# Performance work log

Hardware: AMD Instinct MI355X
Metric: run time of the kernel (lower is better)

## Reference

```python
import jax, jax.numpy as jnp
import numpy as np

T, B, S, H, E, V = 100, 64, 602, 1024, 512, 10000


def setup_inputs() -> dict:
    key = jax.random.key(0)
    ks = jax.random.split(key, 12)
    s = 0.02  # small init scale for numerical stability through tanh/sigmoid
    return {
        "tgt": jax.random.randint(ks[0], (T, B, 1), 0, V),
        "memory_bank": jax.random.normal(ks[1], (S, B, H), jnp.float32),
        "h0": jax.random.normal(ks[2], (2, B, H), jnp.float32) * 0.1,
        "c0": jax.random.normal(ks[3], (2, B, H), jnp.float32) * 0.1,
        "embedding": jax.random.normal(ks[4], (V, E), jnp.float32) * s,
        "Wi0": jax.random.normal(ks[5], (4 * H, E + H), jnp.float32) * s,
        "Wh0": jax.random.normal(ks[6], (4 * H, H), jnp.float32) * s,
        "bi0": jnp.zeros((4 * H,), jnp.float32),
        "bh0": jnp.zeros((4 * H,), jnp.float32),
        "Wi1": jax.random.normal(ks[7], (4 * H, H), jnp.float32) * s,
        "Wh1": jax.random.normal(ks[8], (4 * H, H), jnp.float32) * s,
        "bi1": jnp.zeros((4 * H,), jnp.float32),
        "bh1": jnp.zeros((4 * H,), jnp.float32),
        "W_attn": jax.random.normal(ks[9], (H, H), jnp.float32) * s,
        "W_out": jax.random.normal(ks[10], (H, 2 * H), jnp.float32) * s,
    }


def _lstm_cell(x, h, c, Wi, Wh, bi, bh):
    # PyTorch LSTM gate order: i, f, g, o
    g = x @ Wi.T + h @ Wh.T + bi + bh
    i, f, gg, o = jnp.split(g, 4, axis=-1)
    c2 = jax.nn.sigmoid(f) * c + jax.nn.sigmoid(i) * jnp.tanh(gg)
    h2 = jax.nn.sigmoid(o) * jnp.tanh(c2)
    return h2, c2


def reference(tgt, memory_bank, h0, c0, embedding, Wi0, Wh0, bi0, bh0,
              Wi1, Wh1, bi1, bh1, W_attn, W_out):
    emb = embedding[tgt[:, :, 0]]            # [T, B, E]
    M = jnp.transpose(memory_bank, (1, 0, 2))  # [B, S, H]

    def step(carry, e_t):
        hl0, hl1, cl0, cl1, feed = carry
        x = jnp.concatenate([e_t, feed], axis=-1)        # input feeding
        nh0, nc0 = _lstm_cell(x, hl0, cl0, Wi0, Wh0, bi0, bh0)
        nh1, nc1 = _lstm_cell(nh0, hl1, cl1, Wi1, Wh1, bi1, bh1)
        # GlobalAttention 'general': score = (h W) . m
        q = nh1 @ W_attn.T                                # [B, H]
        align = jnp.einsum('bh,bsh->bs', q, M)            # [B, S]
        a = jax.nn.softmax(align, axis=-1)
        ctx = jnp.einsum('bs,bsh->bh', a, M)              # [B, H]
        out = jnp.tanh(jnp.concatenate([ctx, nh1], -1) @ W_out.T)  # attn_h
        return (nh0, nh1, nc0, nc1, out), (out, a)

    init = (h0[0], h0[1], c0[0], c0[1], jnp.zeros((B, H), emb.dtype))
    (_, _, _, _, _), (outs, attns) = jax.lax.scan(step, init, emb)
    return outs, attns  # [T,B,H], [T,B,S]
```

## Files before the change

kernel.cpp:

```cpp
#include <hip/hip_runtime.h>


#define DI __device__ __forceinline__

typedef __attribute__((ext_vector_type(4))) short s4v;
typedef __attribute__((ext_vector_type(8))) short s8v;
typedef __attribute__((ext_vector_type(4))) float f4v;

DI float b2f(short u) {
  unsigned int x = ((unsigned int)(unsigned short)u) << 16;
  float f; __builtin_memcpy(&f, &x, 4); return f;
}
DI short f2b(float f) {
  unsigned int x; __builtin_memcpy(&x, &f, 4);
  return (short)((x + 0x7fffu + ((x >> 16) & 1u)) >> 16);
}
DI s8v cat8(s4v lo, s4v hi) {
  s8v r; r[0]=lo[0];r[1]=lo[1];r[2]=lo[2];r[3]=lo[3];
  r[4]=hi[0];r[5]=hi[1];r[6]=hi[2];r[7]=hi[3]; return r;
}
DI f4v mfma16(s8v a, s8v b, f4v c) {
  return __builtin_amdgcn_mfma_f32_16x16x32_bf16(a, b, c, 0, 0, 0);
}
DI float sigm(float x) { return 1.f / (1.f + __expf(-x)); }

DI unsigned long long ld64c(const void* p) {
  return __hip_atomic_load((const unsigned long long*)p, __ATOMIC_RELAXED,
                           __HIP_MEMORY_SCOPE_SYSTEM);
}
DI void st64c(void* p, unsigned long long v) {
  __hip_atomic_store((unsigned long long*)p, v, __ATOMIC_RELAXED,
                     __HIP_MEMORY_SCOPE_SYSTEM);
}
DI float ldfc(const float* p) {
  return __hip_atomic_load(p, __ATOMIC_RELAXED, __HIP_MEMORY_SCOPE_SYSTEM);
}
DI void stfc(float* p, float v) {
  __hip_atomic_store(p, v, __ATOMIC_RELAXED, __HIP_MEMORY_SCOPE_SYSTEM);
}
DI void st16c(short* p, short v) {
  asm volatile("global_store_short %0, %1, off sc0 sc1"
               :: "v"(p), "v"((unsigned int)(unsigned short)v) : "memory");
}
union U64S { unsigned long long u; short s[4]; };
union U64F { unsigned long long u; float f[2]; };


__global__ void cvt_bf16(const float* __restrict__ src, short* __restrict__ dst, long n8) {
  long i = (long)blockIdx.x * blockDim.x + threadIdx.x;
  long stride = (long)gridDim.x * blockDim.x;
  for (; i < n8; i += stride) {
    const float* s = src + i * 8;
    s8v o;
    #pragma unroll
    for (int j = 0; j < 8; ++j) o[j] = f2b(s[j]);
    *(s8v*)(dst + i * 8) = o;
  }
}

__global__ void pack_w(const float* __restrict__ WA, int Ka,
                       const float* __restrict__ WB, int Kb,
                       short* __restrict__ dst, int N, long total) {
  long i = (long)blockIdx.x * blockDim.x + threadIdx.x;
  long stride = (long)gridDim.x * blockDim.x;
  for (; i < total; i += stride) {
    int c = (int)(i & 3);
    long r = i >> 2;
    int n = (int)(r % N);
    int kt = (int)(r / N);
    int k = kt * 32 + c * 8;
    const float* s = (k < Ka) ? (WA + (size_t)n * Ka + k)
                              : (WB + (size_t)n * Kb + (k - Ka));
    s8v o;
    #pragma unroll
    for (int j = 0; j < 8; ++j) o[j] = f2b(s[j]);
    *(s8v*)(dst + r * 32 + c * 8) = o;
  }
}

__global__ __launch_bounds__(64) void emb_gather(const int* __restrict__ tgt,
                                                 const float* __restrict__ emb,
                                                 short* __restrict__ dst) {
  int tb = blockIdx.x;
  int idx = tgt[tb];
  const float* s = emb + (size_t)idx * 512 + threadIdx.x * 8;
  s8v o;
  #pragma unroll
  for (int j = 0; j < 8; ++j) o[j] = f2b(s[j]);
  *(s8v*)(dst + (size_t)tb * 512 + threadIdx.x * 8) = o;
}

__global__ void init_state(const float* __restrict__ h0, const float* __restrict__ c0,
                           short* __restrict__ h0r, short* __restrict__ h1r,
                           float* __restrict__ c0buf, float* __restrict__ c1buf,
                           short* __restrict__ feedr) {
  int i = blockIdx.x * 256 + threadIdx.x;
  if (i < 65536) {
    h0r[i] = f2b(h0[i]);
    h1r[i] = f2b(h0[65536 + i]);
    c0buf[i] = c0[i];
    c1buf[i] = c0[65536 + i];
    feedr[i] = 0;
  }
}


template <int K>
DI void stageA(short* As, int rt,
               const short* __restrict__ A0, int ld0, int K0,
               const short* __restrict__ A1, int ld1, int K1,
               const short* __restrict__ A2, int ld2) {
  const int KP = K + 8;
  const int CH = K / 8;
  const int TOT = 16 * CH;
  for (int c = threadIdx.x; c < TOT; c += 256) {
    int row = c / CH, kc = c - row * CH;
    int k = kc * 8;
    int gr = rt * 16 + row;
    const short* p;
    if (k < K0)            p = A0 + (size_t)gr * ld0 + k;
    else if (k < K0 + K1)  p = A1 + (size_t)gr * ld1 + (k - K0);
    else                   p = A2 + (size_t)gr * ld2 + (k - K0 - K1);
    *(s8v*)&As[row * KP + k] = *(const s8v*)p;
  }
}

template <int NG>
DI void kloopL(const short* As, int KP, int k0, int nkt,
               const short* __restrict__ Wp, size_t wkt,
               f4v* acc, int r15, int g) {
  const short* arow = As + r15 * KP + 4 * g;
  #pragma unroll 4
  for (int kt = 0; kt < nkt; ++kt) {
    const short* ap = arow + (k0 + kt) * 32;
    s8v a = cat8(*(const s4v*)ap, *(const s4v*)(ap + 16));
    const short* bp = Wp + (size_t)(k0 + kt) * wkt;
    #pragma unroll
    for (int t = 0; t < NG; ++t)
      acc[t] = mfma16(a, cat8(*(const s4v*)(bp + (size_t)t * 32768),
                              *(const s4v*)(bp + (size_t)t * 32768 + 16)),
                      acc[t]);
  }
}

template <int NG>
DI void wave_reduce(f4v* acc, float* smem, int w, int l) {
  #pragma unroll
  for (int t4 = 0; t4 < NG; ++t4)
    *(f4v*)&smem[(w * 64 + l) * 20 + t4 * 4] = acc[t4];
  __syncthreads();
  if (w == 0) {
    #pragma unroll
    for (int t4 = 0; t4 < NG; ++t4) {
      f4v s0 = *(f4v*)&smem[l * 20 + t4 * 4];
      #pragma unroll
      for (int ww = 1; ww < 4; ++ww) {
        f4v v = *(f4v*)&smem[(ww * 64 + l) * 20 + t4 * 4];
        #pragma unroll
        for (int j = 0; j < 4; ++j) s0[j] += v[j];
      }
      acc[t4] = s0;
    }
  }
}


DI void gbar(int* bar, int bid, int want) {
  __syncthreads();
  if (threadIdx.x == 0) {
    int* leaf = bar + (bid >> 4) * 64;
    if (__hip_atomic_fetch_add(leaf, 1, __ATOMIC_RELAXED,
                               __HIP_MEMORY_SCOPE_AGENT) == want * 16 - 1) {
      if (__hip_atomic_fetch_add(bar + 1024, 1, __ATOMIC_RELAXED,
                                 __HIP_MEMORY_SCOPE_AGENT) == want * 16 - 1) {
        __hip_atomic_store(bar + 1088, want, __ATOMIC_RELAXED,
                           __HIP_MEMORY_SCOPE_AGENT);
      }
    }
    while (__hip_atomic_load(bar + 1088, __ATOMIC_RELAXED,
                             __HIP_MEMORY_SCOPE_AGENT) < want)
      __builtin_amdgcn_s_sleep(2);
  }
  __syncthreads();
}


__global__ __launch_bounds__(256, 1) void decoder_k(
    const short* __restrict__ W0p, const short* __restrict__ W1p,
    const short* __restrict__ Wop, const short* __restrict__ Wap,
    const short* __restrict__ emba,
    const float* __restrict__ bi0, const float* __restrict__ bh0,
    const float* __restrict__ bi1, const float* __restrict__ bh1,
    short* h0r, short* h1r, short* feedr, short* ctxr, short* qb,
    float* c0b, float* c1b, float* alg, float* part,
    const short* __restrict__ Mb, const float* __restrict__ memf,
    float* out, int useMb, int* bar) {
  __shared__ float smem[5248];
  __shared__ __align__(16) short As[16 * 2568];
  const int bid = blockIdx.x, tid = threadIdx.x;
  const int w = tid >> 6, l = tid & 63, r15 = l & 15, g = l >> 4;
  const int cs = bid & 63, rt = bid >> 6;
  int barno = 0;
  f4v z = {0.f, 0.f, 0.f, 0.f};

  for (int t = 0; t < 100; ++t) {
    const size_t scur = (size_t)t * 65536, snxt = (size_t)(t + 1) * 65536;

    {
      f4v acc[4] = {z, z, z, z};
      stageA<2560>(As, rt, emba + (size_t)t * 64 * 512, 512, 512,
                   feedr + scur, 1024, 1024, h0r + scur, 1024);
      __syncthreads();
      const short* wbase = W0p + (size_t)(cs * 16 + r15) * 32 + 4 * g;
      kloopL<4>(As, 2568, w * 20, 20, wbase, (size_t)4096 * 32, acc, r15, g);
      wave_reduce<4>(acc, smem, w, l);
      if (w == 0) {
        int h = cs * 16 + r15;
        float bs0 = bi0[h] + bh0[h];
        float bs1 = bi0[1024 + h] + bh0[1024 + h];
        float bs2 = bi0[2048 + h] + bh0[2048 + h];
        float bs3 = bi0[3072 + h] + bh0[3072 + h];
        #pragma unroll
        for (int q = 0; q < 4; ++q) {
          int brow = rt * 16 + g * 4 + q;
          size_t off = (size_t)brow * 1024 + h;
          float iv = acc[0][q] + bs0, fv = acc[1][q] + bs1;
          float gv = acc[2][q] + bs2, ov = acc[3][q] + bs3;
          float cn = sigm(fv) * c0b[off] + sigm(iv) * tanhf(gv);
          float hn = sigm(ov) * tanhf(cn);
          c0b[off] = cn;
          st16c(h0r + snxt + off, f2b(hn));
        }
      }
      gbar(bar, bid, ++barno);
    }

    {
      f4v acc[4] = {z, z, z, z};
      stageA<2048>(As, rt, h0r + snxt, 1024, 1024, h1r + scur, 1024, 1024,
                   (const short*)nullptr, 0);
      __syncthreads();
      const short* wbase = W1p + (size_t)(cs * 16 + r15) * 32 + 4 * g;
      kloopL<4>(As, 2056, w * 16, 16, wbase, (size_t)4096 * 32, acc, r15, g);
      wave_reduce<4>(acc, smem, w, l);
      if (w == 0) {
        int h = cs * 16 + r15;
        float bs0 = bi1[h] + bh1[h];
        float bs1 = bi1[1024 + h] + bh1[1024 + h];
        float bs2 = bi1[2048 + h] + bh1[2048 + h];
        float bs3 = bi1[3072 + h] + bh1[3072 + h];
        #pragma unroll
        for (int q = 0; q < 4; ++q) {
          int brow = rt * 16 + g * 4 + q;
          size_t off = (size_t)brow * 1024 + h;
          float iv = acc[0][q] + bs0, fv = acc[1][q] + bs1;
          float gv = acc[2][q] + bs2, ov = acc[3][q] + bs3;
          float cn = sigm(fv) * c1b[off] + sigm(iv) * tanhf(gv);
          float hn = sigm(ov) * tanhf(cn);
          c1b[off] = cn;
          st16c(h1r + snxt + off, f2b(hn));
        }
      }
      gbar(bar, bid, ++barno);
    }

    {
      f4v acc[1] = {z};
      stageA<1024>(As, rt, h1r + snxt, 1024, 1024,
                   (const short*)nullptr, 0, 0, (const short*)nullptr, 0);
      __syncthreads();
      const short* wbase = Wap + (size_t)(cs * 16 + r15) * 32 + 4 * g;
      kloopL<1>(As, 1032, w * 8, 8, wbase, (size_t)1024 * 32, acc, r15, g);
      wave_reduce<1>(acc, smem, w, l);
      if (w == 0) {
        int nb = cs * 16 + r15;
        #pragma unroll
        for (int q = 0; q < 4; ++q) {
          int brow = rt * 16 + g * 4 + q;
          st16c(qb + (size_t)brow * 1024 + nb, f2b(acc[0][q]));
        }
      }
      gbar(bar, bid, ++barno);
    }

    {
      int b = bid & 63, chunk = bid >> 6;
      int s0 = chunk * 151;
      int send = 602 < s0 + 151 ? 602 : s0 + 151;
      const short* qp = qb + (size_t)b * 1024 + l * 16;
      float qf[16];
      #pragma unroll
      for (int c4 = 0; c4 < 4; ++c4) {
        U64S x; x.u = ld64c(qp + c4 * 4);
        #pragma unroll
        for (int j = 0; j < 4; ++j) qf[c4 * 4 + j] = b2f(x.s[j]);
      }
      float o[16];
      #pragma unroll
      for (int j = 0; j < 16; ++j) o[j] = 0.f;
      for (int s = s0 + w; s < send; s += 8) {
        int s2 = s + 4;
        bool has2 = s2 < send;
        float mv0[16], mv1[16];
        if (useMb) {
          const short* mp0 = Mb + ((size_t)s * 64 + b) * 1024 + l * 16;
          s8v a0 = *(const s8v*)mp0, a1 = *(const s8v*)(mp0 + 8);
          const short* mp1 = Mb + ((size_t)(has2 ? s2 : s) * 64 + b) * 1024 + l * 16;
          s8v b0 = *(const s8v*)mp1, b1 = *(const s8v*)(mp1 + 8);
          #pragma unroll
          for (int j = 0; j < 8; ++j) {
            mv0[j] = b2f(a0[j]); mv0[8 + j] = b2f(a1[j]);
            mv1[j] = b2f(b0[j]); mv1[8 + j] = b2f(b1[j]);
          }
        } else {
          const float* mp0 = memf + ((size_t)s * 64 + b) * 1024 + l * 16;
          const float* mp1 = memf + ((size_t)(has2 ? s2 : s) * 64 + b) * 1024 + l * 16;
          f4v a0 = *(const f4v*)mp0, a1 = *(const f4v*)(mp0 + 4);
          f4v a2 = *(const f4v*)(mp0 + 8), a3 = *(const f4v*)(mp0 + 12);
          f4v b0 = *(const f4v*)mp1, b1 = *(const f4v*)(mp1 + 4);
          f4v b2 = *(const f4v*)(mp1 + 8), b3 = *(const f4v*)(mp1 + 12);
          #pragma unroll
          for (int j = 0; j < 4; ++j) {
            mv0[j] = a0[j]; mv0[4 + j] = a1[j]; mv0[8 + j] = a2[j]; mv0[12 + j] = a3[j];
            mv1[j] = b0[j]; mv1[4 + j] = b1[j]; mv1[8 + j] = b2[j]; mv1[12 + j] = b3[j];
          }
        }
        float d0 = 0.f, d1 = 0.f;
        #pragma unroll
        for (int j = 0; j < 16; ++j) { d0 += qf[j] * mv0[j]; d1 += qf[j] * mv1[j]; }
        #pragma unroll
        for (int off = 32; off; off >>= 1) {
          d0 += __shfl_down(d0, off);
          d1 += __shfl_down(d1, off);
        }
        d0 = __shfl(d0, 0); d1 = __shfl(d1, 0);
        if (l == 0) {
          stfc(alg + b * 602 + s, d0);
          if (has2) stfc(alg + b * 602 + s2, d1);
        }
        float p0 = __expf(fminf(d0, 80.f) - 8.f);
        float p1 = has2 ? __expf(fminf(d1, 80.f) - 8.f) : 0.f;
        #pragma unroll
        for (int j = 0; j < 16; ++j) o[j] += p0 * mv0[j] + p1 * mv1[j];
      }
      float* pp = part + (size_t)(b * 16 + chunk * 4 + w) * 1024;
      #pragma unroll
      for (int j4 = 0; j4 < 8; ++j4) {
        U64F x; x.f[0] = o[j4 * 2]; x.f[1] = o[j4 * 2 + 1];
        st64c(pp + l * 16 + j4 * 2, x.u);
      }
      gbar(bar, bid, ++barno);
    }

    if (bid < 64) {
      int b = bid;
      float* pv = smem;
      float* red = smem + 604;
      const float* al = alg + b * 602;
      float lm = -1e30f;
      for (int i = tid; i < 602; i += 256) {
        float v = ldfc(al + i); pv[i] = v; lm = fmaxf(lm, v);
      }
      #pragma unroll
      for (int o = 32; o; o >>= 1) lm = fmaxf(lm, __shfl_down(lm, o));
      if (l == 0) red[w] = lm;
      __syncthreads();
      float M = fmaxf(fmaxf(red[0], red[1]), fmaxf(red[2], red[3]));
      float ls = 0.f;
      for (int i = tid; i < 602; i += 256) { float e = __expf(pv[i] - M); pv[i] = e; ls += e; }
      #pragma unroll
      for (int o = 32; o; o >>= 1) ls += __shfl_down(ls, o);
      __syncthreads();
      if (l == 0) red[4 + w] = ls;
      __syncthreads();
      float L = red[4] + red[5] + red[6] + red[7];
      float scale = __expf(8.f - M) / L;
      {
        int h = tid * 4;
        f4v a2 = {0.f, 0.f, 0.f, 0.f};
        #pragma unroll
        for (int p = 0; p < 16; ++p) {
          const float* pr = part + (size_t)(b * 16 + p) * 1024 + h;
          U64F x0, x1; x0.u = ld64c(pr); x1.u = ld64c(pr + 2);
          a2[0] += x0.f[0]; a2[1] += x0.f[1];
          a2[2] += x1.f[0]; a2[3] += x1.f[1];
        }
        U64S ov;
        #pragma unroll
        for (int j = 0; j < 4; ++j) ov.s[j] = f2b(a2[j] * scale);
        st64c(ctxr + snxt + (size_t)b * 1024 + (size_t)tid * 4, ov.u);
      }
      float invL = 1.f / L;
      float* attns = out + 6553600 + (size_t)t * 64 * 602;
      for (int i = tid; i < 602; i += 256) attns[b * 602 + i] = pv[i] * invL;
    }
    gbar(bar, bid, ++barno);

    {
      f4v acc[1] = {z};
      stageA<2048>(As, rt, ctxr + snxt, 1024, 1024, h1r + snxt, 1024, 1024,
                   (const short*)nullptr, 0);
      __syncthreads();
      const short* wbase = Wop + (size_t)(cs * 16 + r15) * 32 + 4 * g;
      kloopL<1>(As, 2056, w * 16, 16, wbase, (size_t)1024 * 32, acc, r15, g);
      wave_reduce<1>(acc, smem, w, l);
      if (w == 0) {
        int nb = cs * 16 + r15;
        float* outp = out + (size_t)t * 65536;
        #pragma unroll
        for (int q = 0; q < 4; ++q) {
          int brow = rt * 16 + g * 4 + q;
          size_t off = (size_t)brow * 1024 + nb;
          float v = tanhf(acc[0][q]);
          outp[off] = v;
          st16c(feedr + snxt + off, f2b(v));
        }
      }
      gbar(bar, bid, ++barno);
    }
  }
}


extern "C" void kernel_launch(void* const* d_in, const int* in_sizes, int n_in,
                              void* d_out, int out_size, void* d_ws, size_t ws_size,
                              hipStream_t stream) {
  const int*   tgt  = (const int*)  d_in[0];
  const float* mem  = (const float*)d_in[1];
  const float* h0   = (const float*)d_in[2];
  const float* c0   = (const float*)d_in[3];
  const float* embw = (const float*)d_in[4];
  const float* Wi0  = (const float*)d_in[5];
  const float* Wh0  = (const float*)d_in[6];
  const float* bi0  = (const float*)d_in[7];
  const float* bh0  = (const float*)d_in[8];
  const float* Wi1  = (const float*)d_in[9];
  const float* Wh1  = (const float*)d_in[10];
  const float* bi1  = (const float*)d_in[11];
  const float* bh1  = (const float*)d_in[12];
  const float* Wat  = (const float*)d_in[13];
  const float* Wou  = (const float*)d_in[14];
  float* out = (float*)d_out;

  char* base = (char*)d_ws;
  size_t off = 0;
  auto alloc = [&](size_t bytes) -> void* {
    void* p = base + off;
    off += (bytes + 255) & ~(size_t)255;
    return p;
  };
  const size_t RING = (size_t)101 * 65536;
  int* bar = (int*)alloc(8192);
  short* qb   = (short*)alloc(65536 * 2);
  float* c0b  = (float*)alloc(65536 * 4);
  float* c1b  = (float*)alloc(65536 * 4);
  float* alg  = (float*)alloc((size_t)64 * 602 * 4);
  float* part = (float*)alloc((size_t)64 * 16 * 1024 * 4);
  short* emba = (short*)alloc((size_t)100 * 64 * 512 * 2);
  short* Wap  = (short*)alloc((size_t)32 * 1024 * 32 * 2);
  short* Wop  = (short*)alloc((size_t)64 * 1024 * 32 * 2);
  short* W1p  = (short*)alloc((size_t)64 * 4096 * 32 * 2);
  short* W0p  = (short*)alloc((size_t)80 * 4096 * 32 * 2);
  short* h0r  = (short*)alloc(RING * 2);
  short* h1r  = (short*)alloc(RING * 2);
  short* feedr= (short*)alloc(RING * 2);
  short* ctxr = (short*)alloc(RING * 2);
  const size_t MBE = (size_t)602 * 64 * 1024;
  bool useMb = (off + MBE * 2 + 256) <= ws_size;
  short* Mb = useMb ? (short*)alloc(MBE * 2) : nullptr;

  hipMemsetAsync(bar, 0, 8192, stream);
  hipLaunchKernelGGL(emb_gather, dim3(6400), dim3(64), 0, stream, tgt, embw, emba);
  hipLaunchKernelGGL(pack_w, dim3(2048), dim3(256), 0, stream, Wi0, 1536, Wh0, 1024,
                     W0p, 4096, (long)80 * 4096 * 4);
  hipLaunchKernelGGL(pack_w, dim3(2048), dim3(256), 0, stream, Wi1, 1024, Wh1, 1024,
                     W1p, 4096, (long)64 * 4096 * 4);
  hipLaunchKernelGGL(pack_w, dim3(1024), dim3(256), 0, stream, Wou, 2048, Wou, 2048,
                     Wop, 1024, (long)64 * 1024 * 4);
  hipLaunchKernelGGL(pack_w, dim3(512), dim3(256), 0, stream, Wat, 1024, Wat, 1024,
                     Wap, 1024, (long)32 * 1024 * 4);
  hipLaunchKernelGGL(init_state, dim3(256), dim3(256), 0, stream, h0, c0,
                     h0r, h1r, c0b, c1b, feedr);
  if (useMb)
    hipLaunchKernelGGL(cvt_bf16, dim3(2048), dim3(256), 0, stream, mem, Mb,
                       (long)(MBE / 8));

  hipLaunchKernelGGL(decoder_k, dim3(256), dim3(256), 0, stream,
                     W0p, W1p, Wop, Wap, emba,
                     bi0, bh0, bi1, bh1,
                     h0r, h1r, feedr, ctxr, qb,
                     c0b, c1b, alg, part,
                     Mb, mem, out, (int)useMb,
                     bar);
}
```

Baseline: 8.140 ms.

## Read GEMM A operands directly from global and replace softmax grid barrier with per-batch counters

```diff
diff --git a/kernel.cpp b/kernel.cpp
--- a/kernel.cpp
+++ b/kernel.cpp
@@ -105,41 +105,64 @@
 }
 
 
-template <int K>
-DI void stageA(short* As, int rt,
-               const short* __restrict__ A0, int ld0, int K0,
-               const short* __restrict__ A1, int ld1, int K1,
-               const short* __restrict__ A2, int ld2) {
-  const int KP = K + 8;
-  const int CH = K / 8;
-  const int TOT = 16 * CH;
-  for (int c = threadIdx.x; c < TOT; c += 256) {
-    int row = c / CH, kc = c - row * CH;
-    int k = kc * 8;
-    int gr = rt * 16 + row;
-    const short* p;
-    if (k < K0)            p = A0 + (size_t)gr * ld0 + k;
-    else if (k < K0 + K1)  p = A1 + (size_t)gr * ld1 + (k - K0);
-    else                   p = A2 + (size_t)gr * ld2 + (k - K0 - K1);
-    *(s8v*)&As[row * KP + k] = *(const s8v*)p;
-  }
-}
-
 template <int NG>
-DI void kloopL(const short* As, int KP, int k0, int nkt,
-               const short* __restrict__ Wp, size_t wkt,
-               f4v* acc, int r15, int g) {
-  const short* arow = As + r15 * KP + 4 * g;
-  #pragma unroll 4
-  for (int kt = 0; kt < nkt; ++kt) {
-    const short* ap = arow + (k0 + kt) * 32;
-    s8v a = cat8(*(const s4v*)ap, *(const s4v*)(ap + 16));
-    const short* bp = Wp + (size_t)(k0 + kt) * wkt;
+DI void kloop(const short* __restrict__ A, int ld, int nkt,
+              const short* __restrict__ Wp, size_t wkt,
+              f4v* acc, int rA, int g) {
+  if (nkt <= 0) return;
+  const short* ap = A + (size_t)rA * ld + 4 * g;
+  s4v alo = *(const s4v*)ap, ahi = *(const s4v*)(ap + 16);
+  s4v blo[NG], bhi[NG];
+  #pragma unroll
+  for (int t = 0; t < NG; ++t) {
+    blo[t] = *(const s4v*)(Wp + (size_t)t * 32768);
+    bhi[t] = *(const s4v*)(Wp + (size_t)t * 32768 + 16);
+  }
+  for (int kt = 0; kt < nkt - 1; ++kt) {
+    const short* apn = ap + (kt + 1) * 32;
+    const short* bpn = Wp + (size_t)(kt + 1) * wkt;
+    s4v nalo = *(const s4v*)apn, nahi = *(const s4v*)(apn + 16);
+    s4v nblo[NG], nbhi[NG];
     #pragma unroll
-    for (int t = 0; t < NG; ++t)
-      acc[t] = mfma16(a, cat8(*(const s4v*)(bp + (size_t)t * 32768),
-                              *(const s4v*)(bp + (size_t)t * 32768 + 16)),
-                      acc[t]);
+    for (int t = 0; t < NG; ++t) {
+      nblo[t] = *(const s4v*)(bpn + (size_t)t * 32768);
+      nbhi[t] = *(const s4v*)(bpn + (size_t)t * 32768 + 16);
+    }
+    s8v a = cat8(alo, ahi);
+    #pragma unroll
+    for (int t = 0; t < NG; ++t) acc[t] = mfma16(a, cat8(blo[t], bhi[t]), acc[t]);
+    alo = nalo; ahi = nahi;
+    #pragma unroll
+    for (int t = 0; t < NG; ++t) { blo[t] = nblo[t]; bhi[t] = nbhi[t]; }
+  }
+  s8v a = cat8(alo, ahi);
+  #pragma unroll
+  for (int t = 0; t < NG; ++t) acc[t] = mfma16(a, cat8(blo[t], bhi[t]), acc[t]);
+}
+
+template <int NG>
+DI void seg_gemm(const short* __restrict__ A0, int ld0, int n0,
+                 const short* __restrict__ A1, int ld1, int n1,
+                 const short* __restrict__ A2, int ld2, int n2,
+                 const short* __restrict__ wbase, size_t wkt,
+                 int k0, int k1, f4v* acc, int rA, int g) {
+  int s = 0;
+  {
+    int a = k0 > s ? k0 : s, b = k1 < (s + n0) ? k1 : (s + n0);
+    if (a < b) kloop<NG>(A0 + (size_t)(a - s) * 32, ld0, b - a,
+                         wbase + (size_t)a * wkt, wkt, acc, rA, g);
+    s += n0;
+  }
+  {
+    int a = k0 > s ? k0 : s, b = k1 < (s + n1) ? k1 : (s + n1);
+    if (a < b) kloop<NG>(A1 + (size_t)(a - s) * 32, ld1, b - a,
+                         wbase + (size_t)a * wkt, wkt, acc, rA, g);
+    s += n1;
+  }
+  if (n2 > 0) {
+    int a = k0 > s ? k0 : s, b = k1 < (s + n2) ? k1 : (s + n2);
+    if (a < b) kloop<NG>(A2 + (size_t)(a - s) * 32, ld2, b - a,
+                         wbase + (size_t)a * wkt, wkt, acc, rA, g);
   }
 }
 
@@ -196,7 +219,6 @@
     const short* __restrict__ Mb, const float* __restrict__ memf,
     float* out, int useMb, int* bar) {
   __shared__ float smem[5248];
-  __shared__ __align__(16) short As[16 * 2568];
   const int bid = blockIdx.x, tid = threadIdx.x;
   const int w = tid >> 6, l = tid & 63, r15 = l & 15, g = l >> 4;
   const int cs = bid & 63, rt = bid >> 6;
@@ -208,11 +230,11 @@
 
     {
       f4v acc[4] = {z, z, z, z};
-      stageA<2560>(As, rt, emba + (size_t)t * 64 * 512, 512, 512,
-                   feedr + scur, 1024, 1024, h0r + scur, 1024);
-      __syncthreads();
       const short* wbase = W0p + (size_t)(cs * 16 + r15) * 32 + 4 * g;
-      kloopL<4>(As, 2568, w * 20, 20, wbase, (size_t)4096 * 32, acc, r15, g);
+      seg_gemm<4>(emba + (size_t)t * 64 * 512, 512, 16,
+                  feedr + scur, 1024, 32, h0r + scur, 1024, 32,
+                  wbase, (size_t)4096 * 32, w * 20, w * 20 + 20,
+                  acc, rt * 16 + r15, g);
       wave_reduce<4>(acc, smem, w, l);
       if (w == 0) {
         int h = cs * 16 + r15;
@@ -237,11 +259,11 @@
 
     {
       f4v acc[4] = {z, z, z, z};
-      stageA<2048>(As, rt, h0r + snxt, 1024, 1024, h1r + scur, 1024, 1024,
-                   (const short*)nullptr, 0);
-      __syncthreads();
       const short* wbase = W1p + (size_t)(cs * 16 + r15) * 32 + 4 * g;
-      kloopL<4>(As, 2056, w * 16, 16, wbase, (size_t)4096 * 32, acc, r15, g);
+      seg_gemm<4>(h0r + snxt, 1024, 32, h1r + scur, 1024, 32,
+                  (const short*)nullptr, 0, 0,
+                  wbase, (size_t)4096 * 32, w * 16, w * 16 + 16,
+                  acc, rt * 16 + r15, g);
       wave_reduce<4>(acc, smem, w, l);
       if (w == 0) {
         int h = cs * 16 + r15;
@@ -266,11 +288,11 @@
 
     {
       f4v acc[1] = {z};
-      stageA<1024>(As, rt, h1r + snxt, 1024, 1024,
-                   (const short*)nullptr, 0, 0, (const short*)nullptr, 0);
-      __syncthreads();
       const short* wbase = Wap + (size_t)(cs * 16 + r15) * 32 + 4 * g;
-      kloopL<1>(As, 1032, w * 8, 8, wbase, (size_t)1024 * 32, acc, r15, g);
+      seg_gemm<1>(h1r + snxt, 1024, 32, (const short*)nullptr, 0, 0,
+                  (const short*)nullptr, 0, 0,
+                  wbase, (size_t)1024 * 32, w * 8, w * 8 + 8,
+                  acc, rt * 16 + r15, g);
       wave_reduce<1>(acc, smem, w, l);
       if (w == 0) {
         int nb = cs * 16 + r15;
@@ -349,60 +371,67 @@
         U64F x; x.f[0] = o[j4 * 2]; x.f[1] = o[j4 * 2 + 1];
         st64c(pp + l * 16 + j4 * 2, x.u);
       }
+      __syncthreads();
+      if (tid == 0) {
+        int* acnt = bar + 2048 + b * 16;
+        __hip_atomic_fetch_add(acnt, 1, __ATOMIC_RELAXED,
+                               __HIP_MEMORY_SCOPE_AGENT);
+        while (__hip_atomic_load(acnt, __ATOMIC_RELAXED,
+                                 __HIP_MEMORY_SCOPE_AGENT) < 4 * (t + 1))
+          __builtin_amdgcn_s_sleep(1);
+      }
+      __syncthreads();
+      {
+        float* pv = smem;
+        float* red = smem + 604;
+        const float* al = alg + b * 602;
+        float lm = -1e30f;
+        for (int i = tid; i < 602; i += 256) {
+          float v = ldfc(al + i); pv[i] = v; lm = fmaxf(lm, v);
+        }
+        #pragma unroll
+        for (int o2 = 32; o2; o2 >>= 1) lm = fmaxf(lm, __shfl_down(lm, o2));
+        if (l == 0) red[w] = lm;
+        __syncthreads();
+        float M = fmaxf(fmaxf(red[0], red[1]), fmaxf(red[2], red[3]));
+        float ls = 0.f;
+        for (int i = tid; i < 602; i += 256) {
+          float e = __expf(pv[i] - M); pv[i] = e; ls += e;
+        }
+        #pragma unroll
+        for (int o2 = 32; o2; o2 >>= 1) ls += __shfl_down(ls, o2);
+        __syncthreads();
+        if (l == 0) red[4 + w] = ls;
+        __syncthreads();
+        float L = red[4] + red[5] + red[6] + red[7];
+        float scale = __expf(8.f - M) / L;
+        if (tid < 128) {
+          int h = chunk * 256 + tid * 2;
+          float a0 = 0.f, a1 = 0.f;
+          #pragma unroll
+          for (int p = 0; p < 16; ++p) {
+            U64F x; x.u = ld64c(part + (size_t)(b * 16 + p) * 1024 + h);
+            a0 += x.f[0]; a1 += x.f[1];
+          }
+          short* cp = ctxr + snxt + (size_t)b * 1024 + h;
+          st16c(cp, f2b(a0 * scale));
+          st16c(cp + 1, f2b(a1 * scale));
+        }
+        float invL = 1.f / L;
+        float* attns = out + 6553600 + (size_t)t * 64 * 602;
+        for (int i = s0 + tid; i < send; i += 256)
+          attns[b * 602 + i] = pv[i] * invL;
+      }
       gbar(bar, bid, ++barno);
     }
-
-    if (bid < 64) {
-      int b = bid;
-      float* pv = smem;
-      float* red = smem + 604;
-      const float* al = alg + b * 602;
-      float lm = -1e30f;
-      for (int i = tid; i < 602; i += 256) {
-        float v = ldfc(al + i); pv[i] = v; lm = fmaxf(lm, v);
-      }
-      #pragma unroll
-      for (int o = 32; o; o >>= 1) lm = fmaxf(lm, __shfl_down(lm, o));
-      if (l == 0) red[w] = lm;
-      __syncthreads();
-      float M = fmaxf(fmaxf(red[0], red[1]), fmaxf(red[2], red[3]));
-      float ls = 0.f;
-      for (int i = tid; i < 602; i += 256) { float e = __expf(pv[i] - M); pv[i] = e; ls += e; }
-      #pragma unroll
-      for (int o = 32; o; o >>= 1) ls += __shfl_down(ls, o);
-      __syncthreads();
-      if (l == 0) red[4 + w] = ls;
-      __syncthreads();
-      float L = red[4] + red[5] + red[6] + red[7];
-      float scale = __expf(8.f - M) / L;
-      {
-        int h = tid * 4;
-        f4v a2 = {0.f, 0.f, 0.f, 0.f};
-        #pragma unroll
-        for (int p = 0; p < 16; ++p) {
-          const float* pr = part + (size_t)(b * 16 + p) * 1024 + h;
-          U64F x0, x1; x0.u = ld64c(pr); x1.u = ld64c(pr + 2);
-          a2[0] += x0.f[0]; a2[1] += x0.f[1];
-          a2[2] += x1.f[0]; a2[3] += x1.f[1];
-        }
-        U64S ov;
-        #pragma unroll
-        for (int j = 0; j < 4; ++j) ov.s[j] = f2b(a2[j] * scale);
-        st64c(ctxr + snxt + (size_t)b * 1024 + (size_t)tid * 4, ov.u);
-      }
-      float invL = 1.f / L;
-      float* attns = out + 6553600 + (size_t)t * 64 * 602;
-      for (int i = tid; i < 602; i += 256) attns[b * 602 + i] = pv[i] * invL;
-    }
-    gbar(bar, bid, ++barno);
 
     {
       f4v acc[1] = {z};
-      stageA<2048>(As, rt, ctxr + snxt, 1024, 1024, h1r + snxt, 1024, 1024,
-                   (const short*)nullptr, 0);
-      __syncthreads();
       const short* wbase = Wop + (size_t)(cs * 16 + r15) * 32 + 4 * g;
-      kloopL<1>(As, 2056, w * 16, 16, wbase, (size_t)1024 * 32, acc, r15, g);
+      seg_gemm<1>(ctxr + snxt, 1024, 32, h1r + snxt, 1024, 32,
+                  (const short*)nullptr, 0, 0,
+                  wbase, (size_t)1024 * 32, w * 16, w * 16 + 16,
+                  acc, rt * 16 + r15, g);
       wave_reduce<1>(acc, smem, w, l);
       if (w == 0) {
         int nb = cs * 16 + r15;
@@ -450,7 +479,7 @@
     return p;
   };
   const size_t RING = (size_t)101 * 65536;
-  int* bar = (int*)alloc(8192);
+  int* bar = (int*)alloc(16384);
   short* qb   = (short*)alloc(65536 * 2);
   float* c0b  = (float*)alloc(65536 * 4);
   float* c1b  = (float*)alloc(65536 * 4);
@@ -469,7 +498,7 @@
   bool useMb = (off + MBE * 2 + 256) <= ws_size;
   short* Mb = useMb ? (short*)alloc(MBE * 2) : nullptr;
 
-  hipMemsetAsync(bar, 0, 8192, stream);
+  hipMemsetAsync(bar, 0, 16384, stream);
   hipLaunchKernelGGL(emb_gather, dim3(6400), dim3(64), 0, stream, tgt, embw, emba);
   hipLaunchKernelGGL(pack_w, dim3(2048), dim3(256), 0, stream, Wi0, 1536, Wh0, 1024,
                      W0p, 4096, (long)80 * 4096 * 4);
```

Measured after the change: 7.787 ms. -4.3%, faster.
